# Performance work log

Hardware: AMD Instinct MI355X
Metric: run time of the kernel (lower is better)

## Reference

```python
import jax, jax.numpy as jnp
import numpy as np

BETA = 0.9
THRESHOLD = 1.0


def setup_inputs() -> dict:
    key = jax.random.key(0)
    k1, k2 = jax.random.split(key)
    T, N_IN, N_OUT = 1024, 4096, 4096
    x = jax.random.normal(k1, (T, N_IN), dtype=jnp.float32)
    # fc1 weight initialized uniform[0,1), shape [out, in] like nn.Linear
    W = jax.random.uniform(k2, (N_OUT, N_IN), dtype=jnp.float32)
    return {"x": x, "W": W}


def reference(x, W):
    # Precompute the batched linear projection over all timesteps: [T, N_OUT]
    cur = jnp.einsum('ti,oi->to', x, W)
    mem0 = jnp.zeros((W.shape[0],), dtype=x.dtype)

    def step(mem, c):
        # snntorch Leaky, reset_mechanism='subtract':
        # reset is computed from the PREVIOUS membrane potential (detached)
        reset = (mem > THRESHOLD).astype(mem.dtype)
        mem_new = BETA * mem + c - reset * THRESHOLD
        spk = (mem_new > THRESHOLD).astype(mem.dtype)
        return mem_new, (spk, mem_new)

    _, (spk_rec, mem_rec) = jax.lax.scan(step, mem0, cur)
    return spk_rec, mem_rec
```

## Files before the change

kernel.cpp:

```cpp
#include <hip/hip_runtime.h>
#include <hip/hip_bf16.h>
#include <stdint.h>


typedef __attribute__((ext_vector_type(8))) short bf16x8;
typedef __attribute__((ext_vector_type(4))) float floatx4;

#define T_STEPS 1024
#define N_IN    4096
#define N_OUT   4096

#define GM 64
#define GN 128
#define BKK 64

#define CHUNK 32
#define NCHUNK (T_STEPS / CHUNK)

#define PH_T 128
#define NB_N 16
#define TP   130

__device__ __forceinline__ unsigned short f2bf_rne(float f) {
    unsigned int u = __builtin_bit_cast(unsigned int, f);
    unsigned int r = 0x7FFFu + ((u >> 16) & 1u);
    return (unsigned short)((u + r) >> 16);
}

__global__ __launch_bounds__(256) void cvt_kernel(const float4* __restrict__ in,
                                                  ushort4* __restrict__ out, int n4) {
    int i = blockIdx.x * blockDim.x + threadIdx.x;
    if (i < n4) {
        float4 v = in[i];
        ushort4 o;
        o.x = f2bf_rne(v.x);
        o.y = f2bf_rne(v.y);
        o.z = f2bf_rne(v.z);
        o.w = f2bf_rne(v.w);
        out[i] = o;
    }
}

__device__ __forceinline__ void gload16(const void* g, void* l) {
    __builtin_amdgcn_global_load_lds((const __attribute__((address_space(1))) void*)g,
                                     (__attribute__((address_space(3))) void*)l,
                                     16, 0, 0);
}

__global__ __launch_bounds__(256) void gemm_bt(const short* __restrict__ A,
                                               const short* __restrict__ B,
                                               float* __restrict__ C) {
    __shared__ short sA[GM * BKK];
    __shared__ short sB[GN * BKK];

    const int tid  = threadIdx.x;
    const int lane = tid & 63;
    const int wv   = tid >> 6;
    const int wn   = wv * 32;

    const int n_tile = blockIdx.x & 31;
    const int m_tile = blockIdx.x >> 5;
    const long bm = (long)m_tile * GM;
    const long bn = (long)n_tile * GN;

    floatx4 acc[4][2] = {};

    const int srow = tid >> 3;
    const int scol = (tid & 7) * 8;
    const short* gA[2];
    const short* gB[4];
    short* lA[2];
    short* lB[4];
#pragma unroll
    for (int p = 0; p < 2; ++p) {
        gA[p] = A + (bm + p * 32 + srow) * (long)N_IN + scol;
        lA[p] = sA + p * 2048 + tid * 8;
    }
#pragma unroll
    for (int p = 0; p < 4; ++p) {
        gB[p] = B + (bn + p * 32 + srow) * (long)N_IN + scol;
        lB[p] = sB + p * 2048 + tid * 8;
    }

    const int fm  = lane & 15;
    const int fko = (lane >> 4) * 8;

    for (int k0 = 0; k0 < N_IN; k0 += BKK) {
#pragma unroll
        for (int p = 0; p < 2; ++p) gload16(gA[p] + k0, lA[p]);
#pragma unroll
        for (int p = 0; p < 4; ++p) gload16(gB[p] + k0, lB[p]);
        __syncthreads();

#pragma unroll
        for (int ks = 0; ks < 2; ++ks) {
            bf16x8 af[4], bfr[2];
#pragma unroll
            for (int i = 0; i < 4; ++i)
                af[i] = *(const bf16x8*)(sA + (i * 16 + fm) * 64 + ks * 32 + fko);
#pragma unroll
            for (int j = 0; j < 2; ++j)
                bfr[j] = *(const bf16x8*)(sB + (wn + j * 16 + fm) * 64 + ks * 32 + fko);
#pragma unroll
            for (int i = 0; i < 4; ++i)
#pragma unroll
                for (int j = 0; j < 2; ++j)
                    acc[i][j] = __builtin_amdgcn_mfma_f32_16x16x32_bf16(
                        af[i], bfr[j], acc[i][j], 0, 0, 0);
        }
        __syncthreads();
    }

    const int cn = lane & 15;
    const int cm = (lane >> 4) * 4;
#pragma unroll
    for (int i = 0; i < 4; ++i)
#pragma unroll
        for (int j = 0; j < 2; ++j)
#pragma unroll
            for (int r = 0; r < 4; ++r)
                C[(bm + i * 16 + cm + r) * (long)N_OUT + bn + wn + j * 16 + cn] =
                    acc[i][j][r];
}

__global__ __launch_bounds__(256) void boundary_kernel(const float* __restrict__ cur,
                                                       float* __restrict__ bnd) {
    __shared__ float ring[2][NB_N * TP];

    const int tid  = threadIdx.x;
    const int wv   = tid >> 6;
    const int lane = tid & 63;
    const int n0   = blockIdx.x * NB_N;

    const int pn = lane & 15;
    const int tr = lane >> 4;

    float mem = 0.0f;

    if (wv < 3) {
        float v[11];
        int gidx[11];
#pragma unroll
        for (int i = 0; i < 11; ++i) {
            int g = wv + 3 * i;
            gidx[i] = g;
            if (g < 32)
                v[i] = cur[(size_t)(g * 4 + tr) * N_OUT + n0 + pn];
        }
#pragma unroll
        for (int i = 0; i < 11; ++i)
            if (gidx[i] < 32)
                ring[0][pn * TP + gidx[i] * 4 + tr] = v[i];
    }
    __syncthreads();

    for (int ph = 0; ph < T_STEPS / PH_T; ++ph) {
        if (wv < 3) {
            if (ph + 1 < T_STEPS / PH_T) {
                const size_t tb = (size_t)(ph + 1) * PH_T;
                float v[11];
                int gidx[11];
#pragma unroll
                for (int i = 0; i < 11; ++i) {
                    int g = wv + 3 * i;
                    gidx[i] = g;
                    if (g < 32)
                        v[i] = cur[(tb + g * 4 + tr) * N_OUT + n0 + pn];
                }
#pragma unroll
                for (int i = 0; i < 11; ++i)
                    if (gidx[i] < 32)
                        ring[(ph + 1) & 1][pn * TP + gidx[i] * 4 + tr] = v[i];
            }
        } else {
            const float* base = &ring[ph & 1][pn * TP];
#pragma unroll
            for (int sub = 0; sub < 4; ++sub) {
                if (lane < 16)
                    bnd[(size_t)(ph * 4 + sub) * N_OUT + n0 + pn] = mem;
                float2 buf[16];
#pragma unroll
                for (int q = 0; q < 16; ++q)
                    buf[q] = *(const float2*)&base[sub * 32 + q * 2];
#pragma unroll
                for (int q = 0; q < 16; ++q) {
                    {
                        float rst = mem > 1.0f ? 1.0f : 0.0f;
                        mem = fmaf(0.9f, mem, buf[q].x) - rst;
                    }
                    {
                        float rst = mem > 1.0f ? 1.0f : 0.0f;
                        mem = fmaf(0.9f, mem, buf[q].y) - rst;
                    }
                }
            }
        }
        __syncthreads();
    }
}

__global__ __launch_bounds__(256) void replay_kernel(const float* __restrict__ cur,
                                                     const float* __restrict__ bnd,
                                                     float* __restrict__ out) {
    const int lane = threadIdx.x & 63;
    const int w    = threadIdx.x >> 6;
    const int n    = blockIdx.x * 64 + lane;
    const int c    = blockIdx.y * 4 + w;
    float* __restrict__ spk  = out;
    float* __restrict__ memo = out + (size_t)T_STEPS * N_OUT;

    float mem = bnd[(size_t)c * N_OUT + n];
    const float* __restrict__ p = cur + (size_t)c * CHUNK * N_OUT + n;

    float v[CHUNK];
#pragma unroll
    for (int j = 0; j < CHUNK; ++j) v[j] = p[(size_t)j * N_OUT];

#pragma unroll
    for (int j = 0; j < CHUNK; ++j) {
        float rst = mem > 1.0f ? 1.0f : 0.0f;
        mem = fmaf(0.9f, mem, v[j]) - rst;
        size_t idx = (size_t)(c * CHUNK + j) * N_OUT + n;
        spk[idx]  = mem > 1.0f ? 1.0f : 0.0f;
        memo[idx] = mem;
    }
}

extern "C" void kernel_launch(void* const* d_in, const int* in_sizes, int n_in,
                              void* d_out, int out_size, void* d_ws, size_t ws_size,
                              hipStream_t stream) {
    const float* x = (const float*)d_in[0];
    const float* W = (const float*)d_in[1];
    float* out = (float*)d_out;

    char* ws = (char*)d_ws;
    const size_t xbBytes = (size_t)T_STEPS * N_IN * 2;
    const size_t WbBytes = (size_t)N_OUT * N_IN * 2;
    const size_t CtBytes = (size_t)T_STEPS * N_OUT * 4;
    short* xb  = (short*)ws;
    short* Wb  = (short*)(ws + xbBytes);
    float* cur = (float*)(ws + xbBytes + WbBytes);
    float* bnd = (float*)(ws + xbBytes + WbBytes + CtBytes);

    {
        int n4 = T_STEPS * N_IN / 4;
        cvt_kernel<<<n4 / 256, 256, 0, stream>>>((const float4*)x, (ushort4*)xb, n4);
    }
    {
        int n4 = N_OUT * N_IN / 4;
        cvt_kernel<<<n4 / 256, 256, 0, stream>>>((const float4*)W, (ushort4*)Wb, n4);
    }

    gemm_bt<<<(N_OUT / GN) * (T_STEPS / GM), 256, 0, stream>>>(xb, Wb, cur);

    boundary_kernel<<<N_OUT / NB_N, 256, 0, stream>>>(cur, bnd);

    replay_kernel<<<dim3(N_OUT / 64, NCHUNK / 4), 256, 0, stream>>>(cur, bnd, out);
}
```

Baseline: 203.5 us.

## Split GEMM K dimension in two and sum partials in scan kernels

Splits the GEMM's reduction dimension into two halves when workspace allows. This doubles the grid from 512 to 1024 blocks so all CUs on the chip get work. The two partial products are written to separate buffers and summed when the boundary and replay kernels load cur. The cost is writing and reading an extra 16MB partial buffer, and the extra loads in the scan kernels.

```diff
diff --git a/kernel.cpp b/kernel.cpp
--- a/kernel.cpp
+++ b/kernel.cpp
@@ -20,6 +20,8 @@
 #define PH_T 128
 #define NB_N 16
 #define TP   130
+
+#define TN ((size_t)T_STEPS * N_OUT)
 
 __device__ __forceinline__ unsigned short f2bf_rne(float f) {
     unsigned int u = __builtin_bit_cast(unsigned int, f);
@@ -49,7 +51,8 @@
 
 __global__ __launch_bounds__(256) void gemm_bt(const short* __restrict__ A,
                                                const short* __restrict__ B,
-                                               float* __restrict__ C) {
+                                               float* __restrict__ P,
+                                               int kLen) {
     __shared__ short sA[GM * BKK];
     __shared__ short sB[GN * BKK];
 
@@ -58,10 +61,15 @@
     const int wv   = tid >> 6;
     const int wn   = wv * 32;
 
-    const int n_tile = blockIdx.x & 31;
-    const int m_tile = blockIdx.x >> 5;
+    const int bid    = blockIdx.x;
+    const int z      = bid >> 9;
+    const int n_tile = bid & 31;
+    const int m_tile = (bid >> 5) & 15;
     const long bm = (long)m_tile * GM;
     const long bn = (long)n_tile * GN;
+    const int kBeg = z * kLen;
+    const int kEnd = kBeg + kLen;
+    float* __restrict__ Pz = P + (size_t)z * TN;
 
     floatx4 acc[4][2] = {};
 
@@ -85,7 +93,7 @@
     const int fm  = lane & 15;
     const int fko = (lane >> 4) * 8;
 
-    for (int k0 = 0; k0 < N_IN; k0 += BKK) {
+    for (int k0 = kBeg; k0 < kEnd; k0 += BKK) {
 #pragma unroll
         for (int p = 0; p < 2; ++p) gload16(gA[p] + k0, lA[p]);
 #pragma unroll
@@ -119,11 +127,12 @@
         for (int j = 0; j < 2; ++j)
 #pragma unroll
             for (int r = 0; r < 4; ++r)
-                C[(bm + i * 16 + cm + r) * (long)N_OUT + bn + wn + j * 16 + cn] =
+                Pz[(bm + i * 16 + cm + r) * (long)N_OUT + bn + wn + j * 16 + cn] =
                     acc[i][j][r];
 }
 
-__global__ __launch_bounds__(256) void boundary_kernel(const float* __restrict__ cur,
+template <int NPART>
+__global__ __launch_bounds__(256) void boundary_kernel(const float* __restrict__ P,
                                                        float* __restrict__ bnd) {
     __shared__ float ring[2][NB_N * TP];
 
@@ -138,19 +147,23 @@
     float mem = 0.0f;
 
     if (wv < 3) {
-        float v[11];
+        float v0[11], v1[11];
         int gidx[11];
 #pragma unroll
         for (int i = 0; i < 11; ++i) {
             int g = wv + 3 * i;
             gidx[i] = g;
-            if (g < 32)
-                v[i] = cur[(size_t)(g * 4 + tr) * N_OUT + n0 + pn];
+            if (g < 32) {
+                size_t idx = (size_t)(g * 4 + tr) * N_OUT + n0 + pn;
+                v0[i] = P[idx];
+                if (NPART == 2) v1[i] = P[TN + idx];
+            }
         }
 #pragma unroll
         for (int i = 0; i < 11; ++i)
             if (gidx[i] < 32)
-                ring[0][pn * TP + gidx[i] * 4 + tr] = v[i];
+                ring[0][pn * TP + gidx[i] * 4 + tr] =
+                    (NPART == 2) ? (v0[i] + v1[i]) : v0[i];
     }
     __syncthreads();
 
@@ -158,19 +171,23 @@
         if (wv < 3) {
             if (ph + 1 < T_STEPS / PH_T) {
                 const size_t tb = (size_t)(ph + 1) * PH_T;
-                float v[11];
+                float v0[11], v1[11];
                 int gidx[11];
 #pragma unroll
                 for (int i = 0; i < 11; ++i) {
                     int g = wv + 3 * i;
                     gidx[i] = g;
-                    if (g < 32)
-                        v[i] = cur[(tb + g * 4 + tr) * N_OUT + n0 + pn];
+                    if (g < 32) {
+                        size_t idx = (tb + g * 4 + tr) * N_OUT + n0 + pn;
+                        v0[i] = P[idx];
+                        if (NPART == 2) v1[i] = P[TN + idx];
+                    }
                 }
 #pragma unroll
                 for (int i = 0; i < 11; ++i)
                     if (gidx[i] < 32)
-                        ring[(ph + 1) & 1][pn * TP + gidx[i] * 4 + tr] = v[i];
+                        ring[(ph + 1) & 1][pn * TP + gidx[i] * 4 + tr] =
+                            (NPART == 2) ? (v0[i] + v1[i]) : v0[i];
             }
         } else {
             const float* base = &ring[ph & 1][pn * TP];
@@ -199,7 +216,8 @@
     }
 }
 
-__global__ __launch_bounds__(256) void replay_kernel(const float* __restrict__ cur,
+template <int NPART>
+__global__ __launch_bounds__(256) void replay_kernel(const float* __restrict__ P,
                                                      const float* __restrict__ bnd,
                                                      float* __restrict__ out) {
     const int lane = threadIdx.x & 63;
@@ -207,14 +225,19 @@
     const int n    = blockIdx.x * 64 + lane;
     const int c    = blockIdx.y * 4 + w;
     float* __restrict__ spk  = out;
-    float* __restrict__ memo = out + (size_t)T_STEPS * N_OUT;
+    float* __restrict__ memo = out + TN;
 
     float mem = bnd[(size_t)c * N_OUT + n];
-    const float* __restrict__ p = cur + (size_t)c * CHUNK * N_OUT + n;
+    const float* __restrict__ p0 = P + (size_t)c * CHUNK * N_OUT + n;
+    const float* __restrict__ p1 = p0 + TN;
 
     float v[CHUNK];
 #pragma unroll
-    for (int j = 0; j < CHUNK; ++j) v[j] = p[(size_t)j * N_OUT];
+    for (int j = 0; j < CHUNK; ++j) {
+        float a = p0[(size_t)j * N_OUT];
+        if (NPART == 2) a += p1[(size_t)j * N_OUT];
+        v[j] = a;
+    }
 
 #pragma unroll
     for (int j = 0; j < CHUNK; ++j) {
@@ -236,11 +259,14 @@
     char* ws = (char*)d_ws;
     const size_t xbBytes = (size_t)T_STEPS * N_IN * 2;
     const size_t WbBytes = (size_t)N_OUT * N_IN * 2;
-    const size_t CtBytes = (size_t)T_STEPS * N_OUT * 4;
-    short* xb  = (short*)ws;
-    short* Wb  = (short*)(ws + xbBytes);
-    float* cur = (float*)(ws + xbBytes + WbBytes);
-    float* bnd = (float*)(ws + xbBytes + WbBytes + CtBytes);
+    const size_t PBytes  = TN * 4;
+    const size_t bndBytes = (size_t)NCHUNK * N_OUT * 4;
+    short* xb = (short*)ws;
+    short* Wb = (short*)(ws + xbBytes);
+    float* P  = (float*)(ws + xbBytes + WbBytes);
+
+    const int S = (ws_size >= xbBytes + WbBytes + 2 * PBytes + bndBytes) ? 2 : 1;
+    float* bnd = (float*)(ws + xbBytes + WbBytes + (size_t)S * PBytes);
 
     {
         int n4 = T_STEPS * N_IN / 4;
@@ -251,9 +277,13 @@
         cvt_kernel<<<n4 / 256, 256, 0, stream>>>((const float4*)W, (ushort4*)Wb, n4);
     }
 
-    gemm_bt<<<(N_OUT / GN) * (T_STEPS / GM), 256, 0, stream>>>(xb, Wb, cur);
-
-    boundary_kernel<<<N_OUT / NB_N, 256, 0, stream>>>(cur, bnd);
-
-    replay_kernel<<<dim3(N_OUT / 64, NCHUNK / 4), 256, 0, stream>>>(cur, bnd, out);
-}
+    gemm_bt<<<512 * S, 256, 0, stream>>>(xb, Wb, P, N_IN / S);
+
+    if (S == 2) {
+        boundary_kernel<2><<<N_OUT / NB_N, 256, 0, stream>>>(P, bnd);
+        replay_kernel<2><<<dim3(N_OUT / 64, NCHUNK / 4), 256, 0, stream>>>(P, bnd, out);
+    } else {
+        boundary_kernel<1><<<N_OUT / NB_N, 256, 0, stream>>>(P, bnd);
+        replay_kernel<1><<<dim3(N_OUT / 64, NCHUNK / 4), 256, 0, stream>>>(P, bnd, out);
+    }
+}
```

Result: no change. 203.2 us (-0.1%).
